# Performance work log

Measured on AMD Instinct MI355X. Metric: run time of the kernel, lower is better.

## Reference

```python
import jax, jax.numpy as jnp
import numpy as np

BATCH, IN_F, OUT_F, GRID_PLUS_ORDER = 8192, 1024, 1024, 8

def setup_inputs() -> dict:
    key = jax.random.key(0)
    k1, k2, k3 = jax.random.split(key, 3)
    x = jax.random.normal(k1, (BATCH, IN_F), dtype=jnp.float32)
    base_weight = jax.random.normal(k2, (OUT_F, IN_F), dtype=jnp.float32) * 0.03
    spline_weight = jax.random.normal(k3, (OUT_F, IN_F, GRID_PLUS_ORDER), dtype=jnp.float32) * 0.1
    return {"x": x, "base_weight": base_weight, "spline_weight": spline_weight}

def reference(x, base_weight, spline_weight):
    # base_output = F.linear(x, base_weight) -> x @ W_b^T
    base_output = x @ base_weight.T  # [B, out]
    # Original: sum_{i,g} silu(x)[b,i] * spline_weight[o,i,g]
    # The grid/order axis g is never contracted with x, so it collapses:
    # silu(x) @ spline_weight.sum(-1).T  -- identical math, no [O,B,I,G] blowup.
    w_spline = jnp.sum(spline_weight, axis=-1)  # [out, in]
    spline_output = jax.nn.silu(x) @ w_spline.T  # [B, out]
    return base_output + spline_output
```

## Files before the change

### kernel.cpp

```cpp
#include <hip/hip_runtime.h>
#include <hip/hip_bf16.h>


#define BATCH 8192
#define IN_F 1024
#define OUT_F 1024
#define KP 2048

typedef unsigned short ushort_t;
typedef __attribute__((ext_vector_type(8))) short short8;
typedef __attribute__((ext_vector_type(4))) float f32x4;

__device__ __forceinline__ ushort_t f2bf(float f) {
  union { float f; unsigned int u; } v;
  v.f = f;
  unsigned int u = v.u;
  u += 0x7fffu + ((u >> 16) & 1u);
  return (ushort_t)(u >> 16);
}

__device__ __forceinline__ void async16(const ushort_t* g, ushort_t* l) {
  __builtin_amdgcn_global_load_lds(
      (const __attribute__((address_space(1))) void*)g,
      (__attribute__((address_space(3))) void*)l, 16, 0, 0);
}

__global__ void prep_x(const float* __restrict__ x, ushort_t* __restrict__ Apack) {
  const int idx = blockIdx.x * 256 + threadIdx.x;
  const int b = idx >> 8;
  const int i = (idx & 255) << 2;
  const float4 xv = *(const float4*)(x + ((size_t)b << 10) + i);

  ushort4 vb;
  vb.x = f2bf(xv.x); vb.y = f2bf(xv.y); vb.z = f2bf(xv.z); vb.w = f2bf(xv.w);

  const float sx = xv.x / (1.0f + __expf(-xv.x));
  const float sy = xv.y / (1.0f + __expf(-xv.y));
  const float sz = xv.z / (1.0f + __expf(-xv.z));
  const float sw = xv.w / (1.0f + __expf(-xv.w));
  ushort4 vs;
  vs.x = f2bf(sx); vs.y = f2bf(sy); vs.z = f2bf(sz); vs.w = f2bf(sw);

  ushort_t* row = Apack + ((size_t)b << 11);
  *(ushort4*)(row + i) = vb;
  *(ushort4*)(row + IN_F + i) = vs;
}

__global__ void prep_w(const float* __restrict__ Wb, const float* __restrict__ Ws,
                       ushort_t* __restrict__ Wpack) {
  const int idx = blockIdx.x * 256 + threadIdx.x;
  const int o = idx >> 11;
  const int k = idx & 2047;
  float v;
  if (k < IN_F) {
    v = Wb[((size_t)o << 10) + k];
  } else {
    const float4* p = (const float4*)(Ws + ((((size_t)o << 10) + (size_t)(k - IN_F)) << 3));
    const float4 a = p[0];
    const float4 b = p[1];
    v = ((a.x + a.y) + (a.z + a.w)) + ((b.x + b.y) + (b.z + b.w));
  }
  Wpack[idx] = f2bf(v);
}

__global__ __launch_bounds__(256) void gemm_packed(
    const ushort_t* __restrict__ A,
    const ushort_t* __restrict__ W,
    float* __restrict__ C) {
  __shared__ ushort_t As[128 * 32];
  __shared__ ushort_t Bs[128 * 32];

  const int t = threadIdx.x;
  const int bx = blockIdx.x;
  const int by = blockIdx.y;

  const int lane = t & 63;
  const int wave = t >> 6;
  const int wr = wave >> 1;
  const int wc = wave & 1;

  const int srow = t >> 2;
  const int scol = (t & 3) << 3;
  const size_t a_g0 = ((size_t)(by * 128 + srow)) * KP + scol;
  const size_t b_g0 = ((size_t)(bx * 128 + srow)) * KP + scol;
  ushort_t* as_d = As + t * 8;
  ushort_t* bs_d = Bs + t * 8;

  f32x4 acc[4][4];
#pragma unroll
  for (int mi = 0; mi < 4; ++mi)
#pragma unroll
    for (int ni = 0; ni < 4; ++ni) acc[mi][ni] = (f32x4){0.f, 0.f, 0.f, 0.f};

  const int arow = wr * 64 + (lane & 15);
  const int brow = wc * 64 + (lane & 15);
  const int kofs = (lane >> 4) << 3;

  for (int k0 = 0; k0 < KP; k0 += 32) {
    __syncthreads();
    async16(A + a_g0 + k0, as_d);
    async16(A + a_g0 + k0 + (size_t)64 * KP, as_d + 2048);
    async16(W + b_g0 + k0, bs_d);
    async16(W + b_g0 + k0 + (size_t)64 * KP, bs_d + 2048);
    __syncthreads();

    short8 af[4], bfr[4];
#pragma unroll
    for (int mi = 0; mi < 4; ++mi)
      af[mi] = *(const short8*)(As + (arow + mi * 16) * 32 + kofs);
#pragma unroll
    for (int ni = 0; ni < 4; ++ni)
      bfr[ni] = *(const short8*)(Bs + (brow + ni * 16) * 32 + kofs);

#pragma unroll
    for (int mi = 0; mi < 4; ++mi)
#pragma unroll
      for (int ni = 0; ni < 4; ++ni)
        acc[mi][ni] = __builtin_amdgcn_mfma_f32_16x16x32_bf16(af[mi], bfr[ni], acc[mi][ni], 0, 0, 0);
  }

  const int col0 = bx * 128 + wc * 64 + (lane & 15);
  const int row0 = by * 128 + wr * 64 + ((lane >> 4) << 2);
#pragma unroll
  for (int mi = 0; mi < 4; ++mi)
#pragma unroll
    for (int ni = 0; ni < 4; ++ni) {
      float* cp = C + (size_t)(row0 + mi * 16) * OUT_F + col0 + ni * 16;
#pragma unroll
      for (int r = 0; r < 4; ++r) cp[(size_t)r * OUT_F] = acc[mi][ni][r];
    }
}

extern "C" void kernel_launch(void* const* d_in, const int* in_sizes, int n_in,
                              void* d_out, int out_size, void* d_ws, size_t ws_size,
                              hipStream_t stream) {
  const float* x = (const float*)d_in[0];
  const float* wb = (const float*)d_in[1];
  const float* ws = (const float*)d_in[2];
  float* out = (float*)d_out;

  ushort_t* Apack = (ushort_t*)d_ws;
  ushort_t* Wpack = (ushort_t*)((char*)d_ws + (size_t)BATCH * KP * sizeof(ushort_t));

  prep_x<<<(BATCH * IN_F / 4) / 256, 256, 0, stream>>>(x, Apack);
  prep_w<<<(OUT_F * KP) / 256, 256, 0, stream>>>(wb, ws, Wpack);
  gemm_packed<<<dim3(OUT_F / 128, BATCH / 128), 256, 0, stream>>>(Apack, Wpack, out);
}
```

Measured before the change: 167.4 us.

## Fuse prep kernels into one launch, vectorize, and remap GEMM tiles per XCD

Merges the x and weight preparation kernels into a single launch that splits work by block range, and widens the loads and stores (8 elements per thread for x, 4 per thread for the weights). It also remaps the GEMM block index so that blocks landing on the same XCD (flat index mod 8) share a group of M tiles, aiming for better L2 reuse of A and W. The costs being targeted are an extra kernel launch, narrow memory accesses, and cross-XCD cache misses. The tile remapping assumes round-robin dispatch of blocks across XCDs.

```diff
diff --git a/kernel.cpp b/kernel.cpp
--- a/kernel.cpp
+++ b/kernel.cpp
@@ -25,42 +25,56 @@
       (__attribute__((address_space(3))) void*)l, 16, 0, 0);
 }
 
-__global__ void prep_x(const float* __restrict__ x, ushort_t* __restrict__ Apack) {
-  const int idx = blockIdx.x * 256 + threadIdx.x;
-  const int b = idx >> 8;
-  const int i = (idx & 255) << 2;
-  const float4 xv = *(const float4*)(x + ((size_t)b << 10) + i);
+#define PREP_A_BLOCKS 4096
+#define PREP_S_BLOCKS 1024
+#define PREP_B_BLOCKS 1024
+#define PREP_BLOCKS (PREP_A_BLOCKS + PREP_S_BLOCKS + PREP_B_BLOCKS)
 
-  ushort4 vb;
-  vb.x = f2bf(xv.x); vb.y = f2bf(xv.y); vb.z = f2bf(xv.z); vb.w = f2bf(xv.w);
+__global__ __launch_bounds__(256) void prep_all(
+    const float* __restrict__ x, const float* __restrict__ Wb,
+    const float* __restrict__ Ws, ushort_t* __restrict__ Apack,
+    ushort_t* __restrict__ Wpack) {
+  const int blk = blockIdx.x;
+  const int t = threadIdx.x;
 
-  const float sx = xv.x / (1.0f + __expf(-xv.x));
-  const float sy = xv.y / (1.0f + __expf(-xv.y));
-  const float sz = xv.z / (1.0f + __expf(-xv.z));
-  const float sw = xv.w / (1.0f + __expf(-xv.w));
-  ushort4 vs;
-  vs.x = f2bf(sx); vs.y = f2bf(sy); vs.z = f2bf(sz); vs.w = f2bf(sw);
-
-  ushort_t* row = Apack + ((size_t)b << 11);
-  *(ushort4*)(row + i) = vb;
-  *(ushort4*)(row + IN_F + i) = vs;
-}
-
-__global__ void prep_w(const float* __restrict__ Wb, const float* __restrict__ Ws,
-                       ushort_t* __restrict__ Wpack) {
-  const int idx = blockIdx.x * 256 + threadIdx.x;
-  const int o = idx >> 11;
-  const int k = idx & 2047;
-  float v;
-  if (k < IN_F) {
-    v = Wb[((size_t)o << 10) + k];
+  if (blk < PREP_A_BLOCKS) {
+    const int idx = blk * 256 + t;
+    const int b = idx >> 7;
+    const int i = (idx & 127) << 3;
+    const float4 x0 = *(const float4*)(x + ((size_t)b << 10) + i);
+    const float4 x1 = *(const float4*)(x + ((size_t)b << 10) + i + 4);
+    float xv[8] = {x0.x, x0.y, x0.z, x0.w, x1.x, x1.y, x1.z, x1.w};
+    ushort_t vb[8], vs[8];
+#pragma unroll
+    for (int j = 0; j < 8; ++j) {
+      vb[j] = f2bf(xv[j]);
+      vs[j] = f2bf(xv[j] / (1.0f + __expf(-xv[j])));
+    }
+    ushort_t* row = Apack + ((size_t)b << 11);
+    *(short8*)(row + i) = *(short8*)vb;
+    *(short8*)(row + IN_F + i) = *(short8*)vs;
+  } else if (blk < PREP_A_BLOCKS + PREP_S_BLOCKS) {
+    const int idx = (blk - PREP_A_BLOCKS) * 256 + t;
+    const int o = idx >> 8;
+    const int i0 = (idx & 255) << 2;
+    ushort_t vs[4];
+#pragma unroll
+    for (int j = 0; j < 4; ++j) {
+      const float4* p = (const float4*)(Ws + ((((size_t)o << 10) + i0 + j) << 3));
+      const float4 a = p[0];
+      const float4 b = p[1];
+      vs[j] = f2bf(((a.x + a.y) + (a.z + a.w)) + ((b.x + b.y) + (b.z + b.w)));
+    }
+    *(ushort4*)(Wpack + ((size_t)o << 11) + IN_F + i0) = *(ushort4*)vs;
   } else {
-    const float4* p = (const float4*)(Ws + ((((size_t)o << 10) + (size_t)(k - IN_F)) << 3));
-    const float4 a = p[0];
-    const float4 b = p[1];
-    v = ((a.x + a.y) + (a.z + a.w)) + ((b.x + b.y) + (b.z + b.w));
+    const int idx = (blk - PREP_A_BLOCKS - PREP_S_BLOCKS) * 256 + t;
+    const int o = idx >> 8;
+    const int c = (idx & 255) << 2;
+    const float4 w = *(const float4*)(Wb + ((size_t)o << 10) + c);
+    ushort4 v;
+    v.x = f2bf(w.x); v.y = f2bf(w.y); v.z = f2bf(w.z); v.w = f2bf(w.w);
+    *(ushort4*)(Wpack + ((size_t)o << 11) + c) = v;
   }
-  Wpack[idx] = f2bf(v);
 }
 
 __global__ __launch_bounds__(256) void gemm_packed(
@@ -71,8 +85,11 @@
   __shared__ ushort_t Bs[128 * 32];
 
   const int t = threadIdx.x;
-  const int bx = blockIdx.x;
-  const int by = blockIdx.y;
+  const int flat = blockIdx.y * 8 + blockIdx.x;
+  const int xcd = flat & 7;
+  const int local = flat >> 3;
+  const int nt = local >> 3;
+  const int mt = xcd * 8 + (local & 7);
 
   const int lane = t & 63;
   const int wave = t >> 6;
@@ -81,8 +98,8 @@
 
   const int srow = t >> 2;
   const int scol = (t & 3) << 3;
-  const size_t a_g0 = ((size_t)(by * 128 + srow)) * KP + scol;
-  const size_t b_g0 = ((size_t)(bx * 128 + srow)) * KP + scol;
+  const size_t a_g0 = ((size_t)(mt * 128 + srow)) * KP + scol;
+  const size_t b_g0 = ((size_t)(nt * 128 + srow)) * KP + scol;
   ushort_t* as_d = As + t * 8;
   ushort_t* bs_d = Bs + t * 8;
 
@@ -119,8 +136,8 @@
         acc[mi][ni] = __builtin_amdgcn_mfma_f32_16x16x32_bf16(af[mi], bfr[ni], acc[mi][ni], 0, 0, 0);
   }
 
-  const int col0 = bx * 128 + wc * 64 + (lane & 15);
-  const int row0 = by * 128 + wr * 64 + ((lane >> 4) << 2);
+  const int col0 = nt * 128 + wc * 64 + (lane & 15);
+  const int row0 = mt * 128 + wr * 64 + ((lane >> 4) << 2);
 #pragma unroll
   for (int mi = 0; mi < 4; ++mi)
 #pragma unroll
@@ -140,9 +157,8 @@
   float* out = (float*)d_out;
 
   ushort_t* Apack = (ushort_t*)d_ws;
-  ushort_t* Wpack = (ushort_t*)((char*)d_ws + (size_t)BATCH * KP * sizeof(ushort_t));
+  ushort_t* Wpack = (ushort_t*)((char*)d_ws + (size_t)BATCH * KP * 2);
 
-  prep_x<<<(BATCH * IN_F / 4) / 256, 256, 0, stream>>>(x, Apack);
-  prep_w<<<(OUT_F * KP) / 256, 256, 0, stream>>>(wb, ws, Wpack);
+  prep_all<<<PREP_BLOCKS, 256, 0, stream>>>(x, wb, ws, Apack, Wpack);
   gemm_packed<<<dim3(OUT_F / 128, BATCH / 128), 256, 0, stream>>>(Apack, Wpack, out);
 }
```

New measurement: 161.7 us. 3.4% less time.
